# Kernel tuning notes

Hardware: AMD Instinct MI355X
Metric: run time of the kernel (lower is better)

Reference implementation:

```python
import jax, jax.numpy as jnp
import numpy as np

NUM_EXPERTS = 4
TOPK = 1
TEMPERATURE = 1.0
NORM_TOPK_PROB = True
N_CLS = 1
N_REL = 4


def setup_inputs() -> dict:
    key = jax.random.key(0)
    ks = jax.random.split(key, 7)
    B, N_total, D, r, E = 64, 1029, 768, 64, NUM_EXPERTS
    x = jax.random.normal(ks[0], (B, N_total, D), dtype=jnp.float32)
    # parameters (torch Linear convention: weight [out, in])
    Wd = jax.random.normal(ks[1], (r, D), dtype=jnp.float32) * (1.0 / np.sqrt(D))
    Wg = jax.random.normal(ks[2], (E, r), dtype=jnp.float32) * (1.0 / np.sqrt(r))
    We = jax.random.normal(ks[3], (E, r, r), dtype=jnp.float32) * (1.0 / np.sqrt(r))
    be = jax.random.normal(ks[4], (E, r), dtype=jnp.float32) * 0.01
    Wu = jax.random.normal(ks[5], (D, r), dtype=jnp.float32) * (1.0 / np.sqrt(r))
    gamma = jnp.ones((D,), dtype=jnp.float32)  # LayerScale init_values=1.0
    return {"x": x, "Wd": Wd, "Wg": Wg, "We": We, "be": be, "Wu": Wu, "gamma": gamma}


def reference(x, Wd, Wg, We, be, Wu, gamma):
    # proj_down (bias=False) + exact GELU (nn.GELU default)
    h = jax.nn.gelu(jnp.einsum('bnd,rd->bnr', x, Wd), approximate=False)  # [B,Nt,r]
    cls_tok = h[:, :N_CLS, :]
    rel_tok = h[:, N_CLS:N_CLS + N_REL, :]
    t = h[:, N_CLS + N_REL:, :]                                           # [B,N,r]
    B, N, r = t.shape

    # gating: softmax scores, top-k selection
    logits = jnp.einsum('bnr,er->bne', t, Wg) / TEMPERATURE
    scores = jax.nn.softmax(logits, axis=-1)                              # [B,N,E]
    topk_w, topk_idx = jax.lax.top_k(scores, TOPK)                        # [B,N,K]
    if TOPK > 1 and NORM_TOPK_PROB:
        topk_w = topk_w / jnp.sum(topk_w, axis=-1, keepdims=True)

    # experts are tiny Linear(r,r): compute all experts densely, then gather.
    # Same math as per-expert gather/GEMM/scatter-combine in the source.
    expert_all = jnp.einsum('bnr,esr->bnes', t, We) + be                  # [B,N,E,r]
    idx_b = jnp.broadcast_to(topk_idx[..., None], (B, N, TOPK, r))
    sel = jnp.take_along_axis(expert_all, idx_b, axis=2)                  # [B,N,K,r]
    combine = jnp.sum(sel * topk_w[..., None], axis=2)                    # [B,N,r]

    full = jnp.concatenate([cls_tok, rel_tok, t + combine], axis=1)       # [B,Nt,r]
    # proj_up (bias=False) + LayerScale
    return jnp.einsum('bnr,dr->bnd', full, Wu) * gamma
```

## Files before the change

kernel.cpp:

```cpp
#include <hip/hip_runtime.h>
#include <math.h>


#define GELU(v) (0.5f*(v)*(1.0f + erff((v)*0.70710678118654752440f)))

__global__ __launch_bounds__(256) void k1_proj_gelu(
    const float* __restrict__ x, const float* __restrict__ Wd,
    float* __restrict__ h)
{
    __shared__ float As[64][68];
    __shared__ float Bs[64][68];
    const int tid = threadIdx.x;
    const int bm  = blockIdx.x;
    const int tm4 = (tid >> 4) << 2;
    const int tn4 = (tid & 15) << 2;
    const float* xblk = x + (size_t)bm * 64 * 768;

    float acc[4][4];
    #pragma unroll
    for (int i = 0; i < 4; ++i)
        #pragma unroll
        for (int j = 0; j < 4; ++j) acc[i][j] = 0.f;

    for (int kt = 0; kt < 768; kt += 64) {
        #pragma unroll
        for (int p = 0; p < 4; ++p) {
            int li = p*1024 + tid*4;
            int m = li >> 6, k = li & 63;
            float4 v = *(const float4*)(xblk + m*768 + kt + k);
            *(float4*)&As[m][k] = v;
        }
        #pragma unroll
        for (int p = 0; p < 4; ++p) {
            int li = p*1024 + tid*4;
            int j = li >> 6, k = li & 63;
            float4 v = *(const float4*)(Wd + j*768 + kt + k);
            int c = j ^ (((k >> 2) & 7) << 2);
            Bs[k+0][c] = v.x; Bs[k+1][c] = v.y; Bs[k+2][c] = v.z; Bs[k+3][c] = v.w;
        }
        __syncthreads();
        #pragma unroll
        for (int kk = 0; kk < 64; kk += 4) {
            const int swz = ((kk >> 2) & 7) << 2;
            float4 av[4], bv[4];
            #pragma unroll
            for (int i = 0; i < 4; ++i) av[i] = *(const float4*)&As[tm4 + i][kk];
            #pragma unroll
            for (int r = 0; r < 4; ++r) bv[r] = *(const float4*)&Bs[kk + r][tn4 ^ swz];
            #pragma unroll
            for (int i = 0; i < 4; ++i) {
                acc[i][0] += av[i].x*bv[0].x; acc[i][1] += av[i].x*bv[0].y;
                acc[i][2] += av[i].x*bv[0].z; acc[i][3] += av[i].x*bv[0].w;
                acc[i][0] += av[i].y*bv[1].x; acc[i][1] += av[i].y*bv[1].y;
                acc[i][2] += av[i].y*bv[1].z; acc[i][3] += av[i].y*bv[1].w;
                acc[i][0] += av[i].z*bv[2].x; acc[i][1] += av[i].z*bv[2].y;
                acc[i][2] += av[i].z*bv[2].z; acc[i][3] += av[i].z*bv[2].w;
                acc[i][0] += av[i].w*bv[3].x; acc[i][1] += av[i].w*bv[3].y;
                acc[i][2] += av[i].w*bv[3].z; acc[i][3] += av[i].w*bv[3].w;
            }
        }
        __syncthreads();
    }
    #pragma unroll
    for (int i = 0; i < 4; ++i) {
        int token = bm*64 + tm4 + i;
        float4 o;
        o.x = GELU(acc[i][0]); o.y = GELU(acc[i][1]);
        o.z = GELU(acc[i][2]); o.w = GELU(acc[i][3]);
        *(float4*)(h + (size_t)token*64 + tn4) = o;
    }
}

__global__ __launch_bounds__(256) void k2_moe(
    const float* __restrict__ Wg, const float* __restrict__ We,
    const float* __restrict__ be, float* __restrict__ h)
{
    __shared__ float sWg[4*64];
    __shared__ float sBe[4*64];
    __shared__ float sWeT[4*64*65];
    __shared__ float sT[4][64];
    const int tid = threadIdx.x;

    for (int i = tid; i < 4*64; i += 256) { sWg[i] = Wg[i]; sBe[i] = be[i]; }
    for (int i = tid; i < 4*64*64; i += 256) {
        int e = i >> 12, rem = i & 4095, s = rem >> 6, k = rem & 63;
        sWeT[(e*64 + k)*65 + s] = We[i];
    }
    __syncthreads();

    const int wv = tid >> 6, lane = tid & 63;
    #pragma unroll 1
    for (int it = 0; it < 16; ++it) {
        int mt = blockIdx.x*64 + wv*16 + it;
        int b = mt >> 10, n = mt & 1023;
        int token = b*1029 + 5 + n;
        float t = h[(size_t)token*64 + lane];

        float l0 = t * sWg[      lane];
        float l1 = t * sWg[ 64 + lane];
        float l2 = t * sWg[128 + lane];
        float l3 = t * sWg[192 + lane];
        #pragma unroll
        for (int off = 32; off > 0; off >>= 1) {
            l0 += __shfl_xor(l0, off);
            l1 += __shfl_xor(l1, off);
            l2 += __shfl_xor(l2, off);
            l3 += __shfl_xor(l3, off);
        }
        int ei = 0; float lm = l0;
        if (l1 > lm) { lm = l1; ei = 1; }
        if (l2 > lm) { lm = l2; ei = 2; }
        if (l3 > lm) { lm = l3; ei = 3; }
        float s = expf(l0 - lm) + expf(l1 - lm) + expf(l2 - lm) + expf(l3 - lm);
        float w = 1.0f / s;

        sT[wv][lane] = t;
        float o = sBe[ei*64 + lane];
        const float* wp = &sWeT[(ei*64)*65 + lane];
        #pragma unroll 8
        for (int k = 0; k < 64; ++k)
            o += sT[wv][k] * wp[k*65];

        h[(size_t)token*64 + lane] = t + w * o;
    }
}

__global__ __launch_bounds__(256) void k3_up_gamma(
    const float* __restrict__ h, const float* __restrict__ Wu,
    const float* __restrict__ gamma, float* __restrict__ out)
{
    __shared__ float Fs[64][68];
    __shared__ float Ws[64][132];
    const int tid = threadIdx.x;
    const int bm = blockIdx.x, bn = blockIdx.y;
    const int tm4 = (tid >> 4) << 2;
    const int tn8 = (tid & 15) << 3;

    #pragma unroll
    for (int p = 0; p < 4; ++p) {
        int li = p*1024 + tid*4;
        int m = li >> 6, k = li & 63;
        *(float4*)&Fs[m][k] = *(const float4*)(h + (size_t)(bm*64 + m)*64 + k);
    }
    #pragma unroll
    for (int p = 0; p < 8; ++p) {
        int li = p*1024 + tid*4;
        int dl = li >> 6, k = li & 63;
        float4 v = *(const float4*)(Wu + (size_t)(bn*128 + dl)*64 + k);
        int c = dl ^ (((k >> 2) & 7) << 2);
        Ws[k+0][c] = v.x; Ws[k+1][c] = v.y; Ws[k+2][c] = v.z; Ws[k+3][c] = v.w;
    }
    __syncthreads();

    float acc[4][8];
    #pragma unroll
    for (int i = 0; i < 4; ++i)
        #pragma unroll
        for (int j = 0; j < 8; ++j) acc[i][j] = 0.f;

    #pragma unroll
    for (int kk = 0; kk < 64; kk += 4) {
        const int swz = ((kk >> 2) & 7) << 2;
        float4 av[4], blo[4], bhi[4];
        #pragma unroll
        for (int i = 0; i < 4; ++i) av[i] = *(const float4*)&Fs[tm4 + i][kk];
        #pragma unroll
        for (int r = 0; r < 4; ++r) {
            blo[r] = *(const float4*)&Ws[kk + r][ tn8      ^ swz];
            bhi[r] = *(const float4*)&Ws[kk + r][(tn8 + 4) ^ swz];
        }
        #pragma unroll
        for (int i = 0; i < 4; ++i) {
            float a0 = av[i].x, a1 = av[i].y, a2 = av[i].z, a3 = av[i].w;
            acc[i][0] += a0*blo[0].x; acc[i][1] += a0*blo[0].y; acc[i][2] += a0*blo[0].z; acc[i][3] += a0*blo[0].w;
            acc[i][4] += a0*bhi[0].x; acc[i][5] += a0*bhi[0].y; acc[i][6] += a0*bhi[0].z; acc[i][7] += a0*bhi[0].w;
            acc[i][0] += a1*blo[1].x; acc[i][1] += a1*blo[1].y; acc[i][2] += a1*blo[1].z; acc[i][3] += a1*blo[1].w;
            acc[i][4] += a1*bhi[1].x; acc[i][5] += a1*bhi[1].y; acc[i][6] += a1*bhi[1].z; acc[i][7] += a1*bhi[1].w;
            acc[i][0] += a2*blo[2].x; acc[i][1] += a2*blo[2].y; acc[i][2] += a2*blo[2].z; acc[i][3] += a2*blo[2].w;
            acc[i][4] += a2*bhi[2].x; acc[i][5] += a2*bhi[2].y; acc[i][6] += a2*bhi[2].z; acc[i][7] += a2*bhi[2].w;
            acc[i][0] += a3*blo[3].x; acc[i][1] += a3*blo[3].y; acc[i][2] += a3*blo[3].z; acc[i][3] += a3*blo[3].w;
            acc[i][4] += a3*bhi[3].x; acc[i][5] += a3*bhi[3].y; acc[i][6] += a3*bhi[3].z; acc[i][7] += a3*bhi[3].w;
        }
    }

    float4 g0 = *(const float4*)(gamma + bn*128 + tn8);
    float4 g1 = *(const float4*)(gamma + bn*128 + tn8 + 4);
    #pragma unroll
    for (int i = 0; i < 4; ++i) {
        int token = bm*64 + tm4 + i;
        float4 o0, o1;
        o0.x = acc[i][0]*g0.x; o0.y = acc[i][1]*g0.y; o0.z = acc[i][2]*g0.z; o0.w = acc[i][3]*g0.w;
        o1.x = acc[i][4]*g1.x; o1.y = acc[i][5]*g1.y; o1.z = acc[i][6]*g1.z; o1.w = acc[i][7]*g1.w;
        float* op = out + (size_t)token*768 + bn*128 + tn8;
        *(float4*)op       = o0;
        *(float4*)(op + 4) = o1;
    }
}

extern "C" void kernel_launch(void* const* d_in, const int* in_sizes, int n_in,
                              void* d_out, int out_size, void* d_ws, size_t ws_size,
                              hipStream_t stream) {
    const float* x     = (const float*)d_in[0];
    const float* Wd    = (const float*)d_in[1];
    const float* Wg    = (const float*)d_in[2];
    const float* We    = (const float*)d_in[3];
    const float* be    = (const float*)d_in[4];
    const float* Wu    = (const float*)d_in[5];
    const float* gamma = (const float*)d_in[6];
    float* out = (float*)d_out;
    float* h   = (float*)d_ws;

    k1_proj_gelu<<<1029, 256, 0, stream>>>(x, Wd, h);
    k2_moe<<<1024, 256, 0, stream>>>(Wg, We, be, h);
    k3_up_gamma<<<dim3(1029, 6), 256, 0, stream>>>(h, Wu, gamma, out);
}
```

Baseline: 518.0 us.

## Move all three GEMM stages to bf16x3 split MFMA matrix cores

Rewrites the down-projection, expert/gating, and up-projection kernels to use 16x16x32 bf16 MFMA instructions. Each fp32 operand is split into high and low bf16 halves, and three products are accumulated to approximate fp32 accuracy. The expert stage now computes all four experts plus the gate logits as one 64x272 GEMM, then selects the chosen expert per token. The up-projection loops over all six column chunks inside one block, reusing the activation tile. This aims to cut the scalar FMA cost, at the price of slightly reduced precision, redundant dense expert computation, and scattered scalar stores.

Measured after the change: 438.8 us. -15.3%, faster.

```diff
diff --git a/kernel.cpp b/kernel.cpp
--- a/kernel.cpp
+++ b/kernel.cpp
@@ -3,71 +3,91 @@
 
 
 #define GELU(v) (0.5f*(v)*(1.0f + erff((v)*0.70710678118654752440f)))
+
+typedef __attribute__((ext_vector_type(8))) short bf16x8;
+typedef __attribute__((ext_vector_type(4))) float f32x4;
+
+#define MFMA(a,b,c) __builtin_amdgcn_mfma_f32_16x16x32_bf16((a),(b),(c),0,0,0)
+
+__device__ __forceinline__ unsigned pk_hi(float a, float b) {
+  return (__float_as_uint(a) >> 16) | (__float_as_uint(b) & 0xFFFF0000u);
+}
+__device__ __forceinline__ float f_lo(float a) {
+  return a - __uint_as_float(__float_as_uint(a) & 0xFFFF0000u);
+}
+__device__ __forceinline__ int swz(int row, int kbyte) {
+  return row*128 + (kbyte ^ ((row & 7) << 4));
+}
+__device__ __forceinline__ void split_store(char* hiB, char* loB, int row, int kg,
+                                            float4 f0, float4 f1) {
+  uint4 hv, lv;
+  hv.x = pk_hi(f0.x, f0.y); hv.y = pk_hi(f0.z, f0.w);
+  hv.z = pk_hi(f1.x, f1.y); hv.w = pk_hi(f1.z, f1.w);
+  lv.x = pk_hi(f_lo(f0.x), f_lo(f0.y)); lv.y = pk_hi(f_lo(f0.z), f_lo(f0.w));
+  lv.z = pk_hi(f_lo(f1.x), f_lo(f1.y)); lv.w = pk_hi(f_lo(f1.z), f_lo(f1.w));
+  int off = swz(row, kg << 4);
+  *(uint4*)(hiB + off) = hv;
+  *(uint4*)(loB + off) = lv;
+}
+__device__ __forceinline__ bf16x8 frag_ld(const char* b, int row, int kbyte) {
+  return *(const bf16x8*)(b + swz(row, kbyte));
+}
 
 __global__ __launch_bounds__(256) void k1_proj_gelu(
     const float* __restrict__ x, const float* __restrict__ Wd,
     float* __restrict__ h)
 {
-    __shared__ float As[64][68];
-    __shared__ float Bs[64][68];
-    const int tid = threadIdx.x;
-    const int bm  = blockIdx.x;
-    const int tm4 = (tid >> 4) << 2;
-    const int tn4 = (tid & 15) << 2;
-    const float* xblk = x + (size_t)bm * 64 * 768;
-
-    float acc[4][4];
-    #pragma unroll
-    for (int i = 0; i < 4; ++i)
-        #pragma unroll
-        for (int j = 0; j < 4; ++j) acc[i][j] = 0.f;
-
-    for (int kt = 0; kt < 768; kt += 64) {
-        #pragma unroll
-        for (int p = 0; p < 4; ++p) {
-            int li = p*1024 + tid*4;
-            int m = li >> 6, k = li & 63;
-            float4 v = *(const float4*)(xblk + m*768 + kt + k);
-            *(float4*)&As[m][k] = v;
-        }
-        #pragma unroll
-        for (int p = 0; p < 4; ++p) {
-            int li = p*1024 + tid*4;
-            int j = li >> 6, k = li & 63;
-            float4 v = *(const float4*)(Wd + j*768 + kt + k);
-            int c = j ^ (((k >> 2) & 7) << 2);
-            Bs[k+0][c] = v.x; Bs[k+1][c] = v.y; Bs[k+2][c] = v.z; Bs[k+3][c] = v.w;
-        }
-        __syncthreads();
-        #pragma unroll
-        for (int kk = 0; kk < 64; kk += 4) {
-            const int swz = ((kk >> 2) & 7) << 2;
-            float4 av[4], bv[4];
-            #pragma unroll
-            for (int i = 0; i < 4; ++i) av[i] = *(const float4*)&As[tm4 + i][kk];
-            #pragma unroll
-            for (int r = 0; r < 4; ++r) bv[r] = *(const float4*)&Bs[kk + r][tn4 ^ swz];
-            #pragma unroll
-            for (int i = 0; i < 4; ++i) {
-                acc[i][0] += av[i].x*bv[0].x; acc[i][1] += av[i].x*bv[0].y;
-                acc[i][2] += av[i].x*bv[0].z; acc[i][3] += av[i].x*bv[0].w;
-                acc[i][0] += av[i].y*bv[1].x; acc[i][1] += av[i].y*bv[1].y;
-                acc[i][2] += av[i].y*bv[1].z; acc[i][3] += av[i].y*bv[1].w;
-                acc[i][0] += av[i].z*bv[2].x; acc[i][1] += av[i].z*bv[2].y;
-                acc[i][2] += av[i].z*bv[2].z; acc[i][3] += av[i].z*bv[2].w;
-                acc[i][0] += av[i].w*bv[3].x; acc[i][1] += av[i].w*bv[3].y;
-                acc[i][2] += av[i].w*bv[3].z; acc[i][3] += av[i].w*bv[3].w;
-            }
-        }
-        __syncthreads();
-    }
-    #pragma unroll
-    for (int i = 0; i < 4; ++i) {
-        int token = bm*64 + tm4 + i;
-        float4 o;
-        o.x = GELU(acc[i][0]); o.y = GELU(acc[i][1]);
-        o.z = GELU(acc[i][2]); o.w = GELU(acc[i][3]);
-        *(float4*)(h + (size_t)token*64 + tn4) = o;
+  __shared__ uint4 AhS[512], AlS[512], BhS[512], BlS[512];
+  char* Ah = (char*)AhS; char* Al = (char*)AlS;
+  char* Bh = (char*)BhS; char* Bl = (char*)BlS;
+  const int tid = threadIdx.x;
+  const int bm  = blockIdx.x;
+  const int wv = tid >> 6, l = tid & 63;
+  const int lg = l >> 4, lr = l & 15;
+  const float* xblk = x + (size_t)bm * (64*768);
+
+  f32x4 acc[4];
+  #pragma unroll
+  for (int i = 0; i < 4; ++i)
+    #pragma unroll
+    for (int j = 0; j < 4; ++j) acc[i][j] = 0.f;
+
+  for (int kt = 0; kt < 768; kt += 64) {
+    #pragma unroll
+    for (int it = 0; it < 2; ++it) {
+      int li = it*256 + tid;
+      int row = li >> 3, kg = li & 7;
+      const float* p = xblk + row*768 + kt + kg*8;
+      float4 f0 = *(const float4*)p, f1 = *(const float4*)(p+4);
+      split_store(Ah, Al, row, kg, f0, f1);
+      const float* q = Wd + row*768 + kt + kg*8;
+      float4 g0 = *(const float4*)q, g1 = *(const float4*)(q+4);
+      split_store(Bh, Bl, row, kg, g0, g1);
+    }
+    __syncthreads();
+    #pragma unroll
+    for (int kc = 0; kc < 2; ++kc) {
+      int kb = kc*64 + lg*16;
+      bf16x8 ah = frag_ld(Ah, wv*16 + lr, kb);
+      bf16x8 al = frag_ld(Al, wv*16 + lr, kb);
+      #pragma unroll
+      for (int nt = 0; nt < 4; ++nt) {
+        bf16x8 bh = frag_ld(Bh, nt*16 + lr, kb);
+        bf16x8 bl = frag_ld(Bl, nt*16 + lr, kb);
+        acc[nt] = MFMA(ah, bh, acc[nt]);
+        acc[nt] = MFMA(ah, bl, acc[nt]);
+        acc[nt] = MFMA(al, bh, acc[nt]);
+      }
+    }
+    __syncthreads();
+  }
+  #pragma unroll
+  for (int nt = 0; nt < 4; ++nt)
+    #pragma unroll
+    for (int r = 0; r < 4; ++r) {
+      int token = bm*64 + wv*16 + lg*4 + r;
+      float v = acc[nt][r];
+      h[(size_t)token*64 + nt*16 + lr] = GELU(v);
     }
 }
 
@@ -75,142 +95,176 @@
     const float* __restrict__ Wg, const float* __restrict__ We,
     const float* __restrict__ be, float* __restrict__ h)
 {
-    __shared__ float sWg[4*64];
-    __shared__ float sBe[4*64];
-    __shared__ float sWeT[4*64*65];
-    __shared__ float sT[4][64];
-    const int tid = threadIdx.x;
-
-    for (int i = tid; i < 4*64; i += 256) { sWg[i] = Wg[i]; sBe[i] = be[i]; }
-    for (int i = tid; i < 4*64*64; i += 256) {
-        int e = i >> 12, rem = i & 4095, s = rem >> 6, k = rem & 63;
-        sWeT[(e*64 + k)*65 + s] = We[i];
-    }
-    __syncthreads();
-
-    const int wv = tid >> 6, lane = tid & 63;
-    #pragma unroll 1
-    for (int it = 0; it < 16; ++it) {
-        int mt = blockIdx.x*64 + wv*16 + it;
-        int b = mt >> 10, n = mt & 1023;
-        int token = b*1029 + 5 + n;
-        float t = h[(size_t)token*64 + lane];
-
-        float l0 = t * sWg[      lane];
-        float l1 = t * sWg[ 64 + lane];
-        float l2 = t * sWg[128 + lane];
-        float l3 = t * sWg[192 + lane];
-        #pragma unroll
-        for (int off = 32; off > 0; off >>= 1) {
-            l0 += __shfl_xor(l0, off);
-            l1 += __shfl_xor(l1, off);
-            l2 += __shfl_xor(l2, off);
-            l3 += __shfl_xor(l3, off);
-        }
-        int ei = 0; float lm = l0;
-        if (l1 > lm) { lm = l1; ei = 1; }
-        if (l2 > lm) { lm = l2; ei = 2; }
-        if (l3 > lm) { lm = l3; ei = 3; }
-        float s = expf(l0 - lm) + expf(l1 - lm) + expf(l2 - lm) + expf(l3 - lm);
-        float w = 1.0f / s;
-
-        sT[wv][lane] = t;
-        float o = sBe[ei*64 + lane];
-        const float* wp = &sWeT[(ei*64)*65 + lane];
-        #pragma unroll 8
-        for (int k = 0; k < 64; ++k)
-            o += sT[wv][k] * wp[k*65];
-
-        h[(size_t)token*64 + lane] = t + w * o;
-    }
+  __shared__ uint4 AhS[512], AlS[512];
+  __shared__ uint4 BhS[2176], BlS[2176];
+  __shared__ float sBe[256];
+  char* Ah = (char*)AhS; char* Al = (char*)AlS;
+  char* Bh = (char*)BhS; char* Bl = (char*)BlS;
+  const int tid = threadIdx.x;
+  const int bm  = blockIdx.x;
+  const int wv = tid >> 6, l = tid & 63;
+  const int lg = l >> 4, lr = l & 15;
+
+  for (int i = tid; i < 2176; i += 256) {
+    int col = i >> 3, kg = i & 7;
+    float4 f0, f1;
+    if (col < 256) {
+      const float* p = We + (size_t)col*64 + kg*8;
+      f0 = *(const float4*)p; f1 = *(const float4*)(p+4);
+    } else if (col < 260) {
+      const float* p = Wg + (col-256)*64 + kg*8;
+      f0 = *(const float4*)p; f1 = *(const float4*)(p+4);
+    } else {
+      f0 = make_float4(0.f,0.f,0.f,0.f); f1 = f0;
+    }
+    split_store(Bh, Bl, col, kg, f0, f1);
+  }
+  sBe[tid] = be[tid];
+  #pragma unroll
+  for (int it = 0; it < 2; ++it) {
+    int li = it*256 + tid;
+    int row = li >> 3, kg = li & 7;
+    int mt = bm*64 + row;
+    int token = (mt >> 10)*1029 + 5 + (mt & 1023);
+    const float* p = h + (size_t)token*64 + kg*8;
+    float4 f0 = *(const float4*)p, f1 = *(const float4*)(p+4);
+    split_store(Ah, Al, row, kg, f0, f1);
+  }
+  __syncthreads();
+
+  f32x4 acc[17];
+  #pragma unroll
+  for (int i = 0; i < 17; ++i)
+    #pragma unroll
+    for (int j = 0; j < 4; ++j) acc[i][j] = 0.f;
+
+  #pragma unroll
+  for (int kc = 0; kc < 2; ++kc) {
+    int kb = kc*64 + lg*16;
+    bf16x8 ah = frag_ld(Ah, wv*16 + lr, kb);
+    bf16x8 al = frag_ld(Al, wv*16 + lr, kb);
+    #pragma unroll
+    for (int nt = 0; nt < 17; ++nt) {
+      bf16x8 bh = frag_ld(Bh, nt*16 + lr, kb);
+      bf16x8 bl = frag_ld(Bl, nt*16 + lr, kb);
+      acc[nt] = MFMA(ah, bh, acc[nt]);
+      acc[nt] = MFMA(ah, bl, acc[nt]);
+      acc[nt] = MFMA(al, bh, acc[nt]);
+    }
+  }
+
+  #pragma unroll
+  for (int r = 0; r < 4; ++r) {
+    float lt = acc[16][r];
+    int base = l & 48;
+    float l0 = __shfl(lt, base + 0);
+    float l1 = __shfl(lt, base + 1);
+    float l2 = __shfl(lt, base + 2);
+    float l3 = __shfl(lt, base + 3);
+    int ei = 0; float lm = l0;
+    if (l1 > lm) { lm = l1; ei = 1; }
+    if (l2 > lm) { lm = l2; ei = 2; }
+    if (l3 > lm) { lm = l3; ei = 3; }
+    float s = expf(l0-lm)+expf(l1-lm)+expf(l2-lm)+expf(l3-lm);
+    float w = 1.0f / s;
+    int mt = bm*64 + wv*16 + lg*4 + r;
+    size_t tbase = (size_t)((mt >> 10)*1029 + 5 + (mt & 1023))*64;
+    #pragma unroll
+    for (int j = 0; j < 4; ++j) {
+      float d0 = acc[j][r], d1 = acc[4+j][r], d2 = acc[8+j][r], d3 = acc[12+j][r];
+      float dsel = d0;
+      dsel = (ei == 1) ? d1 : dsel;
+      dsel = (ei == 2) ? d2 : dsel;
+      dsel = (ei == 3) ? d3 : dsel;
+      int col = j*16 + lr;
+      float bev = sBe[ei*64 + col];
+      float tv = h[tbase + col];
+      h[tbase + col] = tv + w * (dsel + bev);
+    }
+  }
 }
 
 __global__ __launch_bounds__(256) void k3_up_gamma(
     const float* __restrict__ h, const float* __restrict__ Wu,
     const float* __restrict__ gamma, float* __restrict__ out)
 {
-    __shared__ float Fs[64][68];
-    __shared__ float Ws[64][132];
-    const int tid = threadIdx.x;
-    const int bm = blockIdx.x, bn = blockIdx.y;
-    const int tm4 = (tid >> 4) << 2;
-    const int tn8 = (tid & 15) << 3;
-
-    #pragma unroll
-    for (int p = 0; p < 4; ++p) {
-        int li = p*1024 + tid*4;
-        int m = li >> 6, k = li & 63;
-        *(float4*)&Fs[m][k] = *(const float4*)(h + (size_t)(bm*64 + m)*64 + k);
-    }
-    #pragma unroll
-    for (int p = 0; p < 8; ++p) {
-        int li = p*1024 + tid*4;
-        int dl = li >> 6, k = li & 63;
-        float4 v = *(const float4*)(Wu + (size_t)(bn*128 + dl)*64 + k);
-        int c = dl ^ (((k >> 2) & 7) << 2);
-        Ws[k+0][c] = v.x; Ws[k+1][c] = v.y; Ws[k+2][c] = v.z; Ws[k+3][c] = v.w;
+  __shared__ uint4 AhS[512], AlS[512];
+  __shared__ uint4 BhS[1024], BlS[1024];
+  char* Ah = (char*)AhS; char* Al = (char*)AlS;
+  char* Bh = (char*)BhS; char* Bl = (char*)BlS;
+  const int tid = threadIdx.x;
+  const int bm  = blockIdx.x;
+  const int wv = tid >> 6, l = tid & 63;
+  const int lg = l >> 4, lr = l & 15;
+
+  #pragma unroll
+  for (int it = 0; it < 2; ++it) {
+    int li = it*256 + tid;
+    int row = li >> 3, kg = li & 7;
+    const float* p = h + (size_t)(bm*64 + row)*64 + kg*8;
+    float4 f0 = *(const float4*)p, f1 = *(const float4*)(p+4);
+    split_store(Ah, Al, row, kg, f0, f1);
+  }
+
+  for (int c = 0; c < 6; ++c) {
+    if (c) __syncthreads();
+    #pragma unroll
+    for (int it = 0; it < 4; ++it) {
+      int li = it*256 + tid;
+      int row = li >> 3, kg = li & 7;
+      const float* p = Wu + (size_t)(c*128 + row)*64 + kg*8;
+      float4 f0 = *(const float4*)p, f1 = *(const float4*)(p+4);
+      split_store(Bh, Bl, row, kg, f0, f1);
     }
     __syncthreads();
 
-    float acc[4][8];
-    #pragma unroll
-    for (int i = 0; i < 4; ++i)
-        #pragma unroll
-        for (int j = 0; j < 8; ++j) acc[i][j] = 0.f;
-
-    #pragma unroll
-    for (int kk = 0; kk < 64; kk += 4) {
-        const int swz = ((kk >> 2) & 7) << 2;
-        float4 av[4], blo[4], bhi[4];
-        #pragma unroll
-        for (int i = 0; i < 4; ++i) av[i] = *(const float4*)&Fs[tm4 + i][kk];
-        #pragma unroll
-        for (int r = 0; r < 4; ++r) {
-            blo[r] = *(const float4*)&Ws[kk + r][ tn8      ^ swz];
-            bhi[r] = *(const float4*)&Ws[kk + r][(tn8 + 4) ^ swz];
-        }
-        #pragma unroll
-        for (int i = 0; i < 4; ++i) {
-            float a0 = av[i].x, a1 = av[i].y, a2 = av[i].z, a3 = av[i].w;
-            acc[i][0] += a0*blo[0].x; acc[i][1] += a0*blo[0].y; acc[i][2] += a0*blo[0].z; acc[i][3] += a0*blo[0].w;
-            acc[i][4] += a0*bhi[0].x; acc[i][5] += a0*bhi[0].y; acc[i][6] += a0*bhi[0].z; acc[i][7] += a0*bhi[0].w;
-            acc[i][0] += a1*blo[1].x; acc[i][1] += a1*blo[1].y; acc[i][2] += a1*blo[1].z; acc[i][3] += a1*blo[1].w;
-            acc[i][4] += a1*bhi[1].x; acc[i][5] += a1*bhi[1].y; acc[i][6] += a1*bhi[1].z; acc[i][7] += a1*bhi[1].w;
-            acc[i][0] += a2*blo[2].x; acc[i][1] += a2*blo[2].y; acc[i][2] += a2*blo[2].z; acc[i][3] += a2*blo[2].w;
-            acc[i][4] += a2*bhi[2].x; acc[i][5] += a2*bhi[2].y; acc[i][6] += a2*bhi[2].z; acc[i][7] += a2*bhi[2].w;
-            acc[i][0] += a3*blo[3].x; acc[i][1] += a3*blo[3].y; acc[i][2] += a3*blo[3].z; acc[i][3] += a3*blo[3].w;
-            acc[i][4] += a3*bhi[3].x; acc[i][5] += a3*bhi[3].y; acc[i][6] += a3*bhi[3].z; acc[i][7] += a3*bhi[3].w;
-        }
-    }
-
-    float4 g0 = *(const float4*)(gamma + bn*128 + tn8);
-    float4 g1 = *(const float4*)(gamma + bn*128 + tn8 + 4);
-    #pragma unroll
-    for (int i = 0; i < 4; ++i) {
-        int token = bm*64 + tm4 + i;
-        float4 o0, o1;
-        o0.x = acc[i][0]*g0.x; o0.y = acc[i][1]*g0.y; o0.z = acc[i][2]*g0.z; o0.w = acc[i][3]*g0.w;
-        o1.x = acc[i][4]*g1.x; o1.y = acc[i][5]*g1.y; o1.z = acc[i][6]*g1.z; o1.w = acc[i][7]*g1.w;
-        float* op = out + (size_t)token*768 + bn*128 + tn8;
-        *(float4*)op       = o0;
-        *(float4*)(op + 4) = o1;
-    }
+    f32x4 acc[8];
+    #pragma unroll
+    for (int i = 0; i < 8; ++i)
+      #pragma unroll
+      for (int j = 0; j < 4; ++j) acc[i][j] = 0.f;
+
+    #pragma unroll
+    for (int kc = 0; kc < 2; ++kc) {
+      int kb = kc*64 + lg*16;
+      bf16x8 ah = frag_ld(Ah, wv*16 + lr, kb);
+      bf16x8 al = frag_ld(Al, wv*16 + lr, kb);
+      #pragma unroll
+      for (int nt = 0; nt < 8; ++nt) {
+        bf16x8 bh = frag_ld(Bh, nt*16 + lr, kb);
+        bf16x8 bl = frag_ld(Bl, nt*16 + lr, kb);
+        acc[nt] = MFMA(ah, bh, acc[nt]);
+        acc[nt] = MFMA(ah, bl, acc[nt]);
+        acc[nt] = MFMA(al, bh, acc[nt]);
+      }
+    }
+    #pragma unroll
+    for (int nt = 0; nt < 8; ++nt) {
+      int col = c*128 + nt*16 + lr;
+      float gv = gamma[col];
+      #pragma unroll
+      for (int r = 0; r < 4; ++r) {
+        int token = bm*64 + wv*16 + lg*4 + r;
+        out[(size_t)token*768 + col] = acc[nt][r] * gv;
+      }
+    }
+  }
 }
 
 extern "C" void kernel_launch(void* const* d_in, const int* in_sizes, int n_in,
                               void* d_out, int out_size, void* d_ws, size_t ws_size,
                               hipStream_t stream) {
-    const float* x     = (const float*)d_in[0];
-    const float* Wd    = (const float*)d_in[1];
-    const float* Wg    = (const float*)d_in[2];
-    const float* We    = (const float*)d_in[3];
-    const float* be    = (const float*)d_in[4];
-    const float* Wu    = (const float*)d_in[5];
-    const float* gamma = (const float*)d_in[6];
-    float* out = (float*)d_out;
-    float* h   = (float*)d_ws;
-
-    k1_proj_gelu<<<1029, 256, 0, stream>>>(x, Wd, h);
-    k2_moe<<<1024, 256, 0, stream>>>(Wg, We, be, h);
-    k3_up_gamma<<<dim3(1029, 6), 256, 0, stream>>>(h, Wu, gamma, out);
-}
+  const float* x     = (const float*)d_in[0];
+  const float* Wd    = (const float*)d_in[1];
+  const float* Wg    = (const float*)d_in[2];
+  const float* We    = (const float*)d_in[3];
+  const float* be    = (const float*)d_in[4];
+  const float* Wu    = (const float*)d_in[5];
+  const float* gamma = (const float*)d_in[6];
+  float* out = (float*)d_out;
+  float* h   = (float*)d_ws;
+
+  k1_proj_gelu<<<1029, 256, 0, stream>>>(x, Wd, h);
+  k2_moe<<<1024, 256, 0, stream>>>(Wg, We, be, h);
+  k3_up_gamma<<<1029, 256, 0, stream>>>(h, Wu, gamma, out);
+}
```
